# Kernel tuning notes

Hardware: AMD Instinct MI355X
Metric: run time of the kernel (lower is better)

Reference implementation:

```python
import jax, jax.numpy as jnp
import numpy as np

T, B, H1 = 256, 8, 512
U, H2 = 64, 512
V = 128


def setup_inputs() -> dict:
    key = jax.random.key(0)
    k1, k2, k3, k4, k5, k6 = jax.random.split(key, 6)
    f = jax.random.normal(k1, (T, B, H1), dtype=jnp.float32)
    g = jax.random.normal(k2, (B, U, H2), dtype=jnp.float32)
    f_lens = jax.random.randint(k3, (B,), 1, T + 1)
    g_lens = jax.random.randint(k4, (B,), 1, U + 1)
    W = jax.random.normal(k5, (H1 + H2, V), dtype=jnp.float32) * (1.0 / np.sqrt(H1 + H2))
    b = jax.random.normal(k6, (V,), dtype=jnp.float32) * 0.01
    return {"f": f, "f_lens": f_lens, "g": g, "g_lens": g_lens, "W": W, "b": b}


def reference(f, f_lens, g, g_lens, W, b):
    # Original: f [T,B,H1] -> [B,T,1,H1] expand, g [B,U,H2] -> [B,1,U,H2] expand,
    # concat on last dim -> [B,T,U,H1+H2], then Linear over last dim.
    # Linear(concat) == f @ W[:H1] + g @ W[H1:] + b, broadcast-summed -- same math,
    # without materializing the [B,T,U,H1+H2] intermediate.
    Wf, Wg = W[:H1], W[H1:]
    pf = jnp.einsum('tbh,hv->btv', f, Wf)          # [B,T,V]
    pg = jnp.einsum('buh,hv->buv', g, Wg)          # [B,U,V]
    h = pf[:, :, None, :] + pg[:, None, :, :] + b  # [B,T,U,V]
    return h, f_lens
```

## Files before the change

kernel.cpp:

```cpp
#include <hip/hip_runtime.h>
#include <hip/hip_bf16.h>


typedef float  f32x4 __attribute__((ext_vector_type(4)));
typedef short  bh8   __attribute__((ext_vector_type(8)));

__device__ __forceinline__ unsigned short f2bf(float x) {
    unsigned u = __float_as_uint(x);
    return (unsigned short)((u + 0x7FFFu + ((u >> 16) & 1u)) >> 16);
}

__device__ __forceinline__ bh8 cvt8(f32x4 a, f32x4 b) {
    bh8 r;
    r[0] = (short)f2bf(a[0]); r[1] = (short)f2bf(a[1]);
    r[2] = (short)f2bf(a[2]); r[3] = (short)f2bf(a[3]);
    r[4] = (short)f2bf(b[0]); r[5] = (short)f2bf(b[1]);
    r[6] = (short)f2bf(b[2]); r[7] = (short)f2bf(b[3]);
    return r;
}

__global__ __launch_bounds__(256) void proj4(const float* __restrict__ F,
                                             const float* __restrict__ G,
                                             const float* __restrict__ W,
                                             float* __restrict__ P) {
    __shared__ float sred[4][16][128];

    const int tid = threadIdx.x;
    const int rows16 = blockIdx.x * 16;
    const bool isF = rows16 < 2048;
    const int koff = isF ? 0 : 512;
    const int w = tid >> 6, lane = tid & 63, l15 = lane & 15, cc = lane >> 4;

    const int rr = rows16 + l15;
    const float* arow = isF ? F + (((rr & 255) << 3) + (rr >> 8)) * 512
                            : G + (rr - 2048) * 512;

    f32x4 acc[8] = {};
#pragma unroll
    for (int kk = 0; kk < 4; ++kk) {
        const int k0 = w * 128 + kk * 32 + cc * 8;
        f32x4 a0 = *reinterpret_cast<const f32x4*>(arow + k0);
        f32x4 a1 = *reinterpret_cast<const f32x4*>(arow + k0 + 4);
        bh8 av = cvt8(a0, a1);
#pragma unroll
        for (int j = 0; j < 8; ++j) {
            const float* wsrc = W + (koff + k0) * 128 + (j * 16 + l15);
            bh8 bv;
#pragma unroll
            for (int i = 0; i < 8; ++i) bv[i] = (short)f2bf(wsrc[i * 128]);
            acc[j] = __builtin_amdgcn_mfma_f32_16x16x32_bf16(av, bv, acc[j], 0, 0, 0);
        }
    }
#pragma unroll
    for (int j = 0; j < 8; ++j)
#pragma unroll
        for (int q = 0; q < 4; ++q)
            sred[w][cc * 4 + q][j * 16 + l15] = acc[j][q];
    __syncthreads();

    const int row = tid >> 4, colq = tid & 15;
    f32x4 s0 = {}, s1 = {};
#pragma unroll
    for (int ww = 0; ww < 4; ++ww) {
        s0 += *reinterpret_cast<const f32x4*>(&sred[ww][row][colq * 8]);
        s1 += *reinterpret_cast<const f32x4*>(&sred[ww][row][colq * 8 + 4]);
    }
    float* pdst = P + (rows16 + row) * 128 + colq * 8;
    *reinterpret_cast<f32x4*>(pdst)     = s0;
    *reinterpret_cast<f32x4*>(pdst + 4) = s1;
}

__global__ __launch_bounds__(256) void bcast(const float* __restrict__ P,
                                             const float* __restrict__ bias,
                                             const int* __restrict__ f_lens,
                                             float* __restrict__ out,
                                             int lens_off) {
    const int r   = blockIdx.x;
    const int tid = threadIdx.x;
    const int b   = r >> 8;
    const int vq  = tid & 31;
    const int u0  = tid >> 5;

    f32x4 pf = *reinterpret_cast<const f32x4*>(P + r * 128 + vq * 4);
    f32x4 bi = *reinterpret_cast<const f32x4*>(bias + vq * 4);
    pf += bi;

    const float* pg = P + (2048 + b * 64) * 128;
    float* ob = out + (size_t)r * 8192;

#pragma unroll
    for (int i = 0; i < 8; ++i) {
        int u = u0 * 8 + i;
        f32x4 v = *reinterpret_cast<const f32x4*>(pg + u * 128 + vq * 4);
        v += pf;
        *reinterpret_cast<f32x4*>(ob + u * 128 + vq * 4) = v;
    }

    if (r == 0 && tid < 8) out[lens_off + tid] = (float)f_lens[tid];
}

extern "C" void kernel_launch(void* const* d_in, const int* in_sizes, int n_in,
                              void* d_out, int out_size, void* d_ws, size_t ws_size,
                              hipStream_t stream) {
    const float* f      = (const float*)d_in[0];
    const int*   f_lens = (const int*)  d_in[1];
    const float* g      = (const float*)d_in[2];
    const float* W      = (const float*)d_in[4];
    const float* bias   = (const float*)d_in[5];
    float* out = (float*)d_out;

    float* P = (float*)d_ws;

    proj4<<<dim3(160),  dim3(256), 0, stream>>>(f, g, W, P);
    bcast<<<dim3(2048), dim3(256), 0, stream>>>(P, bias, f_lens, out, out_size - 8);
}
```

Before: 23.80 us.

## Split projection columns across waves instead of K to drop LDS reduction

Each wave now computes a 32-column slice of the projection over the full K range instead of a K-quarter over all 128 columns. This removes the shared-memory partial-sum buffer, the block barrier and the cross-wave reduction, and each wave stores its results to the workspace directly. In exchange, every wave reads the full A row, so A traffic within a block is four times redundant, and the dependent MFMA chain per accumulator is longer.

Measured after the change: 26.39 us. +10.8%, slower.

```diff
diff --git a/kernel.cpp b/kernel.cpp
--- a/kernel.cpp
+++ b/kernel.cpp
@@ -19,12 +19,10 @@
     return r;
 }
 
-__global__ __launch_bounds__(256) void proj4(const float* __restrict__ F,
+__global__ __launch_bounds__(256) void proj5(const float* __restrict__ F,
                                              const float* __restrict__ G,
                                              const float* __restrict__ W,
                                              float* __restrict__ P) {
-    __shared__ float sred[4][16][128];
-
     const int tid = threadIdx.x;
     const int rows16 = blockIdx.x * 16;
     const bool isF = rows16 < 2048;
@@ -34,40 +32,30 @@
     const int rr = rows16 + l15;
     const float* arow = isF ? F + (((rr & 255) << 3) + (rr >> 8)) * 512
                             : G + (rr - 2048) * 512;
+    const int c0 = w * 32;
 
-    f32x4 acc[8] = {};
-#pragma unroll
-    for (int kk = 0; kk < 4; ++kk) {
-        const int k0 = w * 128 + kk * 32 + cc * 8;
+    f32x4 acc[2] = {};
+#pragma unroll 4
+    for (int kk = 0; kk < 16; ++kk) {
+        const int k0 = kk * 32 + cc * 8;
         f32x4 a0 = *reinterpret_cast<const f32x4*>(arow + k0);
         f32x4 a1 = *reinterpret_cast<const f32x4*>(arow + k0 + 4);
         bh8 av = cvt8(a0, a1);
 #pragma unroll
-        for (int j = 0; j < 8; ++j) {
-            const float* wsrc = W + (koff + k0) * 128 + (j * 16 + l15);
+        for (int jj = 0; jj < 2; ++jj) {
+            const float* wsrc = W + (koff + k0) * 128 + (c0 + jj * 16 + l15);
             bh8 bv;
 #pragma unroll
             for (int i = 0; i < 8; ++i) bv[i] = (short)f2bf(wsrc[i * 128]);
-            acc[j] = __builtin_amdgcn_mfma_f32_16x16x32_bf16(av, bv, acc[j], 0, 0, 0);
+            acc[jj] = __builtin_amdgcn_mfma_f32_16x16x32_bf16(av, bv, acc[jj], 0, 0, 0);
         }
     }
+
 #pragma unroll
-    for (int j = 0; j < 8; ++j)
+    for (int jj = 0; jj < 2; ++jj)
 #pragma unroll
         for (int q = 0; q < 4; ++q)
-            sred[w][cc * 4 + q][j * 16 + l15] = acc[j][q];
-    __syncthreads();
-
-    const int row = tid >> 4, colq = tid & 15;
-    f32x4 s0 = {}, s1 = {};
-#pragma unroll
-    for (int ww = 0; ww < 4; ++ww) {
-        s0 += *reinterpret_cast<const f32x4*>(&sred[ww][row][colq * 8]);
-        s1 += *reinterpret_cast<const f32x4*>(&sred[ww][row][colq * 8 + 4]);
-    }
-    float* pdst = P + (rows16 + row) * 128 + colq * 8;
-    *reinterpret_cast<f32x4*>(pdst)     = s0;
-    *reinterpret_cast<f32x4*>(pdst + 4) = s1;
+            P[(rows16 + cc * 4 + q) * 128 + c0 + jj * 16 + l15] = acc[jj][q];
 }
 
 __global__ __launch_bounds__(256) void bcast(const float* __restrict__ P,
@@ -111,6 +99,6 @@
 
     float* P = (float*)d_ws;
 
-    proj4<<<dim3(160),  dim3(256), 0, stream>>>(f, g, W, P);
+    proj5<<<dim3(160),  dim3(256), 0, stream>>>(f, g, W, P);
     bcast<<<dim3(2048), dim3(256), 0, stream>>>(P, bias, f_lens, out, out_size - 8);
 }
```
